# Optimization experiments

Hardware: AMD Instinct MI355X
Metric: run time of the kernel (lower is better)

## Reference

```python
import jax, jax.numpy as jnp
import numpy as np

D, T, B, DEPTH, WIN, H = 1024, 2048, 4, 2, 128, 4
HD = D // H


def setup_inputs() -> dict:
    key = jax.random.key(0)
    ks = iter(jax.random.split(key, 32))
    s = D ** -0.5
    inp = {
        'x': jax.random.normal(next(ks), (B, T, D), jnp.float32),
        'ln1_s': jnp.ones((DEPTH, D)), 'ln1_b': jnp.zeros((DEPTH, D)),
        'ln2_s': jnp.ones((DEPTH, D)), 'ln2_b': jnp.zeros((DEPTH, D)),
        'ln3_s': jnp.ones((DEPTH, D)), 'ln3_b': jnp.zeros((DEPTH, D)),
        'rg_in_w': jax.random.normal(next(ks), (DEPTH, D, D)) * s,
        'rg_in_b': jnp.zeros((DEPTH, D)),
        'rg_gate_w': jax.random.normal(next(ks), (DEPTH, D, D)) * s,
        'rg_gate_b': jnp.zeros((DEPTH, D)),
        'rg_out_w': jax.random.normal(next(ks), (DEPTH, D, D)) * s,
        'rg_out_b': jnp.zeros((DEPTH, D)),
        'qkv_w': jax.random.normal(next(ks), (DEPTH, D, 3 * D)) * s,
        'qkv_b': jnp.zeros((DEPTH, 3 * D)),
        'attn_out_w': jax.random.normal(next(ks), (DEPTH, D, D)) * s,
        'attn_out_b': jnp.zeros((DEPTH, D)),
        'mlp_w1': jax.random.normal(next(ks), (DEPTH, D, 4 * D)) * s,
        'mlp_b1': jnp.zeros((DEPTH, 4 * D)),
        'mlp_w2': jax.random.normal(next(ks), (DEPTH, 4 * D, D)) * (4 * D) ** -0.5,
        'mlp_b2': jnp.zeros((DEPTH, D)),
    }
    return inp


def _ln(x, s, b):
    m = x.mean(-1, keepdims=True)
    v = ((x - m) ** 2).mean(-1, keepdims=True)
    return (x - m) / jnp.sqrt(v + 1e-5) * s + b


def _rg_lru(x, wi, bi, wg, bg, wo, bo):
    u = x @ wi + bi                      # [B,T,D]
    g = jax.nn.sigmoid(x @ wg + bg)      # [B,T,D]
    # h_t = g_t * h_{t-1} + (1-g_t) * u_t, h_{-1}=0 -> log-depth associative scan
    def comb(l, r):
        return (l[0] * r[0], r[0] * l[1] + r[1])
    _, h = jax.lax.associative_scan(comb, (g, (1.0 - g) * u), axis=1)
    return h @ wo + bo


def _local_attn(x, wqkv, bqkv, wo, bo):
    b, t, d = x.shape
    qkv = (x @ wqkv + bqkv).reshape(b, t, 3, H, HD)
    qkv = jnp.transpose(qkv, (2, 0, 3, 1, 4))  # [3,B,H,T,hd]
    q, k, v = qkv[0], qkv[1], qkv[2]
    scores = jnp.einsum('bhid,bhjd->bhij', q, k) / (HD ** 0.5)
    i = jnp.arange(t)[:, None]
    j = jnp.arange(t)[None, :]
    mask = (j <= i) & (j >= i - (WIN - 1))
    scores = jnp.where(mask, scores, -jnp.inf)
    p = jax.nn.softmax(scores, axis=-1)
    y = jnp.einsum('bhij,bhjd->bhid', p, v)
    y = jnp.transpose(y, (0, 2, 1, 3)).reshape(b, t, d)
    return y @ wo + bo


def reference(x, ln1_s, ln1_b, ln2_s, ln2_b, ln3_s, ln3_b,
              rg_in_w, rg_in_b, rg_gate_w, rg_gate_b, rg_out_w, rg_out_b,
              qkv_w, qkv_b, attn_out_w, attn_out_b,
              mlp_w1, mlp_b1, mlp_w2, mlp_b2):
    for l in range(DEPTH):
        x = x + _rg_lru(_ln(x, ln1_s[l], ln1_b[l]),
                        rg_in_w[l], rg_in_b[l], rg_gate_w[l], rg_gate_b[l],
                        rg_out_w[l], rg_out_b[l])
        x = x + _local_attn(_ln(x, ln2_s[l], ln2_b[l]),
                            qkv_w[l], qkv_b[l], attn_out_w[l], attn_out_b[l])
        h = _ln(x, ln3_s[l], ln3_b[l])
        h = jax.nn.gelu(h @ mlp_w1[l] + mlp_b1[l], approximate=False) @ mlp_w2[l] + mlp_b2[l]
        x = x + h
    return x
```

## Files before the change

### kernel.cpp

```cpp
#include <hip/hip_runtime.h>
#include <math.h>

#define DD 1024
#define TT 2048
#define BB 4
#define HH 4
#define HDIM 256
#define NLAYER 2
#define MM (BB*TT)
#define NCHUNK 32
#define CHUNK (TT/NCHUNK)

typedef unsigned short u16;
typedef __bf16 bf16x8 __attribute__((ext_vector_type(8)));
typedef float f32x4 __attribute__((ext_vector_type(4)));

__device__ __forceinline__ float b2f(u16 h) {
  unsigned u = ((unsigned)h) << 16;
  return __builtin_bit_cast(float, u);
}
__device__ __forceinline__ u16 f2b(float f) {
  unsigned u = __builtin_bit_cast(unsigned, f);
  u += 0x7fffu + ((u >> 16) & 1u);
  return (u16)(u >> 16);
}

#define GLD16(g, l) __builtin_amdgcn_global_load_lds( \
    (__attribute__((address_space(1))) void*)(void*)(g), \
    (__attribute__((address_space(3))) void*)(l), 16, 0, 0)

__device__ __forceinline__ void wg_barrier() {
  asm volatile("" ::: "memory");
  __builtin_amdgcn_s_barrier();
  asm volatile("" ::: "memory");
}
template<int N> __device__ __forceinline__ void wait_vmcnt() {
  asm volatile("s_waitcnt vmcnt(%0)" :: "i"(N) : "memory");
}

__global__ __launch_bounds__(256)
void transpose_cvt(const float* __restrict__ W, u16* __restrict__ Wt, int K, int N,
                   size_t lsrc, size_t ldst) {
  __shared__ float tile[32][33];
  const float* Wl = W + (size_t)blockIdx.z * lsrc;
  u16* Wtl = Wt + (size_t)blockIdx.z * ldst;
  const int n0 = blockIdx.x << 5, k0 = blockIdx.y << 5;
  const int tx = threadIdx.x, ty = threadIdx.y;
#pragma unroll
  for (int i = 0; i < 4; ++i)
    tile[ty + i*8][tx] = Wl[(size_t)(k0 + ty + i*8) * N + n0 + tx];
  __syncthreads();
#pragma unroll
  for (int i = 0; i < 4; ++i)
    Wtl[(size_t)(n0 + ty + i*8) * K + k0 + tx] = f2b(tile[tx][ty + i*8]);
}

__global__ __launch_bounds__(256)
void ln_k(const float* __restrict__ x, const float* __restrict__ sc,
          const float* __restrict__ bi, u16* __restrict__ xn) {
  const int row = blockIdx.x;
  const int tid = threadIdx.x;
  const float4 xv = ((const float4*)(x + (size_t)row * DD))[tid];
  float s = xv.x + xv.y + xv.z + xv.w;
  float q = xv.x*xv.x + xv.y*xv.y + xv.z*xv.z + xv.w*xv.w;
#pragma unroll
  for (int o = 1; o < 64; o <<= 1) { s += __shfl_xor(s, o); q += __shfl_xor(q, o); }
  __shared__ float rs[4], rq[4];
  if ((tid & 63) == 0) { rs[tid >> 6] = s; rq[tid >> 6] = q; }
  __syncthreads();
  s = rs[0] + rs[1] + rs[2] + rs[3];
  q = rq[0] + rq[1] + rq[2] + rq[3];
  const float mean = s * (1.f / DD);
  const float var = q * (1.f / DD) - mean * mean;
  const float rstd = rsqrtf(var + 1e-5f);
  const float4 sv = ((const float4*)sc)[tid];
  const float4 bv = ((const float4*)bi)[tid];
  const u16 o0 = f2b((xv.x - mean) * rstd * sv.x + bv.x);
  const u16 o1 = f2b((xv.y - mean) * rstd * sv.y + bv.y);
  const u16 o2 = f2b((xv.z - mean) * rstd * sv.z + bv.z);
  const u16 o3 = f2b((xv.w - mean) * rstd * sv.w + bv.w);
  uint2 pk;
  pk.x = (unsigned)o0 | ((unsigned)o1 << 16);
  pk.y = (unsigned)o2 | ((unsigned)o3 << 16);
  *(uint2*)(xn + (size_t)row * DD + (tid << 2)) = pk;
}

template<int EPI>
__global__ __launch_bounds__(512, 4)
void gemm256t(const u16* __restrict__ A, const u16* __restrict__ Wt,
              const float* __restrict__ bias, const float* __restrict__ bias2,
              float* __restrict__ outf, u16* __restrict__ outb, int K, int N) {
  extern __shared__ u16 lds[];
  const int tid = threadIdx.x;
  const int gx = gridDim.x;
  const int nwg = gx * (int)gridDim.y;
  int lid = (int)blockIdx.y * gx + (int)blockIdx.x;
  lid = (lid & 7) * (nwg >> 3) + (lid >> 3);
  const int m0 = (lid / gx) << 8;
  const int n0 = (lid % gx) << 7;
  const int lane = tid & 63;
  const int wid = tid >> 6;
  const int wm = wid >> 2;
  const int wn = wid & 3;
  const int g = lane >> 4;
  const int lc = lane & 15;
  const int q = tid >> 2;
  const int slot = tid & 3;
  const int scs = (slot ^ ((q >> 1) & 3)) << 3;
  const int so = (g ^ ((lc >> 1) & 3)) << 3;

  u16* Ab = lds;
  u16* Bbase = lds + 24576;
  u16 *Ac = Ab, *An = Ab + 8192, *Aw = Ab + 16384;
  u16 *Bc = Bbase, *Bn = Bbase + 4096, *Bw = Bbase + 8192;

  auto stage = [&](int kt, u16* At, u16* Bt) {
    const int kb = (kt << 5) + scs;
    GLD16(A + (size_t)(m0 + q) * K + kb,       At + q*32 + slot*8);
    GLD16(A + (size_t)(m0 + 128 + q) * K + kb, At + (128 + q)*32 + slot*8);
    GLD16(Wt + (size_t)(n0 + q) * K + kb,      Bt + q*32 + slot*8);
  };

  f32x4 acc[8][2];
#pragma unroll
  for (int i = 0; i < 8; ++i)
#pragma unroll
    for (int j = 0; j < 2; ++j)
#pragma unroll
      for (int e = 0; e < 4; ++e) acc[i][j][e] = 0.f;

  const int KT = K >> 5;
  stage(0, Ac, Bc);
  stage(1, An, Bn);

  for (int kt = 0; kt < KT; ++kt) {
    if (kt + 1 < KT) wait_vmcnt<3>();
    else             wait_vmcnt<0>();
    wg_barrier();
    bf16x8 bf0 = *(const bf16x8*)(Bc + (wn*32 + lc)*32 + so);
    bf16x8 bf1 = *(const bf16x8*)(Bc + (wn*32 + 16 + lc)*32 + so);
    bf16x8 af[8];
#pragma unroll
    for (int i = 0; i < 8; ++i)
      af[i] = *(const bf16x8*)(Ac + (wm*128 + i*16 + lc)*32 + so);
    if (kt + 2 < KT) stage(kt + 2, Aw, Bw);
    __builtin_amdgcn_s_setprio(1);
#pragma unroll
    for (int i = 0; i < 8; ++i) {
      acc[i][0] = __builtin_amdgcn_mfma_f32_16x16x32_bf16(af[i], bf0, acc[i][0], 0, 0, 0);
      acc[i][1] = __builtin_amdgcn_mfma_f32_16x16x32_bf16(af[i], bf1, acc[i][1], 0, 0, 0);
    }
    __builtin_amdgcn_s_setprio(0);
    u16* t;
    t = Ac; Ac = An; An = Aw; Aw = t;
    t = Bc; Bc = Bn; Bn = Bw; Bw = t;
  }

#pragma unroll
  for (int mi = 0; mi < 8; ++mi) {
#pragma unroll
    for (int ni = 0; ni < 2; ++ni) {
      const int n = n0 + wn*32 + ni*16 + lc;
      const int mbase = m0 + wm*128 + mi*16 + (g << 2);
      if (EPI == 4) {
        const float bia = bias[n];
        if (n < 2048) {
#pragma unroll
          for (int e = 0; e < 4; ++e)
            outb[(size_t)(mbase + e) * 2048 + n] = f2b(acc[mi][ni][e] + bia);
        } else {
          const int hh = (n - 2048) >> 8, dim = (n - 2048) & 255;
          const int bidx = mbase >> 11, t = mbase & 2047;
          const u16 a0 = f2b(acc[mi][ni][0] + bia);
          const u16 a1 = f2b(acc[mi][ni][1] + bia);
          const u16 a2 = f2b(acc[mi][ni][2] + bia);
          const u16 a3 = f2b(acc[mi][ni][3] + bia);
          uint2 pk;
          pk.x = (unsigned)a0 | ((unsigned)a1 << 16);
          pk.y = (unsigned)a2 | ((unsigned)a3 << 16);
          u16* vtp = (u16*)outf;
          *(uint2*)(vtp + ((size_t)((bidx*4 + hh)*256 + dim)) * 2048 + t) = pk;
        }
      } else if (EPI == 5) {
        const float bia = (n < 1024) ? bias[n] : bias2[n - 1024];
        u16* dst = (n < 1024) ? outb : (u16*)outf;
        const int nn = n & 1023;
#pragma unroll
        for (int e = 0; e < 4; ++e)
          dst[(size_t)(mbase + e) * 1024 + nn] = f2b(acc[mi][ni][e] + bia);
      } else if (EPI == 2) {
        const float bia = bias[n];
#pragma unroll
        for (int e = 0; e < 4; ++e) {
          const float v = acc[mi][ni][e] + bia;
          const float zc = fminf(fmaxf(1.5957691216f * (v + 0.044715f*v*v*v), -30.f), 30.f);
          outb[(size_t)(mbase + e) * N + n] = f2b(v / (1.f + __expf(-zc)));
        }
      } else {
        const float bia = bias[n];
#pragma unroll
        for (int e = 0; e < 4; ++e)
          outf[(size_t)(mbase + e) * N + n] += acc[mi][ni][e] + bia;
      }
    }
  }
}

__global__ __launch_bounds__(256)
void scan1_k(const u16* __restrict__ zpre, const u16* __restrict__ u,
             float* __restrict__ aggA, float* __restrict__ aggB) {
  const int d = blockIdx.x * 256 + threadIdx.x;
  const int c = blockIdx.y, b = blockIdx.z;
  const size_t base = ((size_t)b * TT + (size_t)c * CHUNK) * DD + d;
  float a = 1.f, acc = 0.f;
  for (int t = 0; t < CHUNK; ++t) {
    const float gl = 1.f / (1.f + __expf(-b2f(zpre[base + (size_t)t * DD])));
    const float ul = b2f(u[base + (size_t)t * DD]);
    acc = gl * acc + (1.f - gl) * ul;
    a *= gl;
  }
  const size_t o = ((size_t)b * NCHUNK + c) * DD + d;
  aggA[o] = a; aggB[o] = acc;
}

__global__ __launch_bounds__(256)
void scan2_k(const float* __restrict__ aggA, const float* __restrict__ aggB,
             float* __restrict__ carry) {
  const int idx = blockIdx.x * 256 + threadIdx.x;
  const int b = idx >> 10, d = idx & 1023;
  float h = 0.f;
  for (int c = 0; c < NCHUNK; ++c) {
    const size_t o = ((size_t)b * NCHUNK + c) * DD + d;
    carry[o] = h;
    h = aggA[o] * h + aggB[o];
  }
}

__global__ __launch_bounds__(256)
void scan3_k(const u16* __restrict__ zpre, const u16* __restrict__ u,
             const float* __restrict__ carry, u16* __restrict__ hout) {
  const int d = blockIdx.x * 256 + threadIdx.x;
  const int c = blockIdx.y, b = blockIdx.z;
  const size_t base = ((size_t)b * TT + (size_t)c * CHUNK) * DD + d;
  float h = carry[((size_t)b * NCHUNK + c) * DD + d];
  for (int t = 0; t < CHUNK; ++t) {
    const float gl = 1.f / (1.f + __expf(-b2f(zpre[base + (size_t)t * DD])));
    const float ul = b2f(u[base + (size_t)t * DD]);
    h = gl * h + (1.f - gl) * ul;
    hout[base + (size_t)t * DD] = f2b(h);
  }
}

__global__ __launch_bounds__(256)
void attn_mfma(const u16* __restrict__ qkb, const u16* __restrict__ vt,
               u16* __restrict__ y) {
  __shared__ u16 kv[16384];
  __shared__ u16 pb[4][16][200];
  const int tid = threadIdx.x;
  const int lane = tid & 63;
  const int wid = tid >> 6;
  const int g = lane >> 4;
  const int lc = lane & 15;
  const int t0 = blockIdx.x << 6;
  const int bh = blockIdx.y;
  const int bT = (bh >> 2) * TT;
  const int h = bh & 3;

  bf16x8 afq[8];
  {
    const u16* qg = qkb + (size_t)(bT + t0 + wid*16 + lc) * 2048 + h*256 + g*8;
#pragma unroll
    for (int ks = 0; ks < 8; ++ks)
      afq[ks] = __builtin_bit_cast(bf16x8, *(const uint4*)(qg + ks*32));
  }

  f32x4 sc[12];
#pragma unroll
  for (int f = 0; f < 12; ++f)
#pragma unroll
    for (int e = 0; e < 4; ++e) sc[f][e] = 0.f;

  const int koff = 1024 + h*256;
#pragma unroll
  for (int c = 0; c < 3; ++c) {
    const int j0 = t0 + (c - 2) * 64;
    if (j0 < 0) {
#pragma unroll
      for (int nt = 0; nt < 4; ++nt)
#pragma unroll
        for (int e = 0; e < 4; ++e) sc[c*4+nt][e] = -1e30f;
      continue;
    }
    __syncthreads();
    {
      const u16* kg = qkb + (size_t)(bT + j0) * 2048 + koff;
#pragma unroll
      for (int i = 0; i < 8; ++i) {
        const int o16 = i*256 + tid;
        const int slab = o16 >> 8, key = (o16 >> 2) & 63, ds = o16 & 3;
        GLD16(kg + (size_t)key*2048 + slab*32 + ds*8, kv + o16*8);
      }
    }
    __syncthreads();
#pragma unroll
    for (int nt = 0; nt < 4; ++nt) {
      f32x4 s = sc[c*4+nt];
#pragma unroll
      for (int ks = 0; ks < 8; ++ks) {
        const bf16x8 kb = *(const bf16x8*)(kv + ks*2048 + (nt*16 + lc)*32 + g*8);
        s = __builtin_amdgcn_mfma_f32_16x16x32_bf16(afq[ks], kb, s, 0, 0, 0);
      }
      sc[c*4+nt] = s;
    }
#pragma unroll
    for (int nt = 0; nt < 4; ++nt)
#pragma unroll
      for (int e = 0; e < 4; ++e) {
        const int tl = wid*16 + g*4 + e;
        const int jl = nt*16 + lc;
        const bool ok = (c == 1) || (c == 2 ? (jl <= tl) : (jl >= tl + 1));
        sc[c*4+nt][e] = ok ? sc[c*4+nt][e] * 0.0625f : -1e30f;
      }
  }

#pragma unroll
  for (int e = 0; e < 4; ++e) {
    float m = -1e30f;
#pragma unroll
    for (int f = 0; f < 12; ++f) m = fmaxf(m, sc[f][e]);
    m = fmaxf(m, __shfl_xor(m, 1)); m = fmaxf(m, __shfl_xor(m, 2));
    m = fmaxf(m, __shfl_xor(m, 4)); m = fmaxf(m, __shfl_xor(m, 8));
    float s = 0.f;
#pragma unroll
    for (int f = 0; f < 12; ++f) { const float p = __expf(sc[f][e] - m); sc[f][e] = p; s += p; }
    s += __shfl_xor(s, 1); s += __shfl_xor(s, 2);
    s += __shfl_xor(s, 4); s += __shfl_xor(s, 8);
    const float is = 1.f / s;
#pragma unroll
    for (int f = 0; f < 12; ++f) sc[f][e] *= is;
  }
#pragma unroll
  for (int c = 0; c < 3; ++c)
#pragma unroll
    for (int nt = 0; nt < 4; ++nt)
#pragma unroll
      for (int e = 0; e < 4; ++e)
        pb[wid][g*4 + e][c*64 + nt*16 + lc] = f2b(sc[c*4+nt][e]);

  f32x4 acc[16];
#pragma unroll
  for (int nt = 0; nt < 16; ++nt)
#pragma unroll
    for (int e = 0; e < 4; ++e) acc[nt][e] = 0.f;

  const u16* vg = vt + (size_t)bh * 256 * 2048;
#pragma unroll
  for (int c = 0; c < 3; ++c) {
    const int j0 = t0 + (c - 2) * 64;
    if (j0 < 0) continue;
    __syncthreads();
#pragma unroll
    for (int i = 0; i < 8; ++i) {
      const int o16 = i*256 + tid;
      const int dim = o16 >> 3, slot = o16 & 7;
      const int ss = slot ^ (dim & 7);
      GLD16(vg + (size_t)dim*2048 + j0 + ss*8, kv + o16*8);
    }
    __syncthreads();
#pragma unroll
    for (int ks = 0; ks < 2; ++ks) {
      const bf16x8 pa = *(const bf16x8*)&pb[wid][lc][(c*2 + ks)*32 + g*8];
#pragma unroll
      for (int nt = 0; nt < 16; ++nt) {
        const int dim = nt*16 + lc;
        int boff = dim*128 + ks*64 + g*16;
        boff ^= (dim & 7) << 4;
        const bf16x8 vb = *(const bf16x8*)((const char*)kv + boff);
        acc[nt] = __builtin_amdgcn_mfma_f32_16x16x32_bf16(pa, vb, acc[nt], 0, 0, 0);
      }
    }
  }

#pragma unroll
  for (int nt = 0; nt < 16; ++nt)
#pragma unroll
    for (int e = 0; e < 4; ++e) {
      const int tok = bT + t0 + wid*16 + g*4 + e;
      y[(size_t)tok * 1024 + h*256 + nt*16 + lc] = f2b(acc[nt][e]);
    }
}

extern "C" void kernel_launch(void* const* d_in, const int* in_sizes, int n_in,
                              void* d_out, int out_size, void* d_ws, size_t ws_size,
                              hipStream_t stream) {
  const float* x_in      = (const float*)d_in[0];
  const float* ln1_s     = (const float*)d_in[1];
  const float* ln1_b     = (const float*)d_in[2];
  const float* ln2_s     = (const float*)d_in[3];
  const float* ln2_b     = (const float*)d_in[4];
  const float* ln3_s     = (const float*)d_in[5];
  const float* ln3_b     = (const float*)d_in[6];
  const float* rg_in_w   = (const float*)d_in[7];
  const float* rg_in_b   = (const float*)d_in[8];
  const float* rg_gate_w = (const float*)d_in[9];
  const float* rg_gate_b = (const float*)d_in[10];
  const float* rg_out_w  = (const float*)d_in[11];
  const float* rg_out_b  = (const float*)d_in[12];
  const float* qkv_w     = (const float*)d_in[13];
  const float* qkv_b     = (const float*)d_in[14];
  const float* attn_out_w= (const float*)d_in[15];
  const float* attn_out_b= (const float*)d_in[16];
  const float* mlp_w1    = (const float*)d_in[17];
  const float* mlp_b1    = (const float*)d_in[18];
  const float* mlp_w2    = (const float*)d_in[19];
  const float* mlp_b2    = (const float*)d_in[20];

  hipFuncSetAttribute((const void*)&gemm256t<5>, hipFuncAttributeMaxDynamicSharedMemorySize, 73728);
  hipFuncSetAttribute((const void*)&gemm256t<4>, hipFuncAttributeMaxDynamicSharedMemorySize, 73728);
  hipFuncSetAttribute((const void*)&gemm256t<2>, hipFuncAttributeMaxDynamicSharedMemorySize, 73728);
  hipFuncSetAttribute((const void*)&gemm256t<3>, hipFuncAttributeMaxDynamicSharedMemorySize, 73728);

  float* x = (float*)d_out;
  char* ws = (char*)d_ws;
  u16*  wt     = (u16*)ws;
  u16*  xn     = (u16*)(ws + 62914560);
  char* bigS   = ws + 62914560 + 16777216;
  char* smallS = bigS + 67108864;
  float* aggA  = (float*)(smallS + 16777216);
  float* aggB  = aggA + (size_t)BB * NCHUNK * DD;
  float* carry = aggB + (size_t)BB * NCHUNK * DD;

  u16* ubuf = (u16*)bigS;
  u16* zbuf = (u16*)(bigS + 33554432);
  u16* qkb  = (u16*)bigS;
  u16* vtb  = (u16*)(bigS + 33554432);
  u16* hid  = (u16*)bigS;
  u16* hbuf = (u16*)smallS;
  u16* ybuf = (u16*)smallS;

  hipMemcpyAsync(x, x_in, (size_t)MM * DD * sizeof(float), hipMemcpyDeviceToDevice, stream);

  const size_t LW = 15728640;
  const dim3 tb(32, 8);
  transpose_cvt<<<dim3(32, 32, 2),  tb, 0, stream>>>(rg_in_w,    wt + 0,        DD, DD,   DD*DD,   LW);
  transpose_cvt<<<dim3(32, 32, 2),  tb, 0, stream>>>(rg_gate_w,  wt + 1048576,  DD, DD,   DD*DD,   LW);
  transpose_cvt<<<dim3(32, 32, 2),  tb, 0, stream>>>(rg_out_w,   wt + 2097152,  DD, DD,   DD*DD,   LW);
  transpose_cvt<<<dim3(96, 32, 2),  tb, 0, stream>>>(qkv_w,      wt + 3145728,  DD, 3072, DD*3072, LW);
  transpose_cvt<<<dim3(32, 32, 2),  tb, 0, stream>>>(attn_out_w, wt + 6291456,  DD, DD,   DD*DD,   LW);
  transpose_cvt<<<dim3(128, 32, 2), tb, 0, stream>>>(mlp_w1,     wt + 7340032,  DD, 4096, DD*4096, LW);
  transpose_cvt<<<dim3(32, 128, 2), tb, 0, stream>>>(mlp_w2,     wt + 11534336, 4096, DD, 4096*DD, LW);

  for (int l = 0; l < NLAYER; ++l) {
    u16* base = wt + (size_t)l * LW;
    ln_k<<<MM, 256, 0, stream>>>(x, ln1_s + l*DD, ln1_b + l*DD, xn);
    gemm256t<5><<<dim3(16, 32), 512, 73728, stream>>>(xn, base + 0, rg_in_b + l*DD, rg_gate_b + l*DD,
                                                      (float*)zbuf, ubuf, DD, 2048);
    scan1_k<<<dim3(4, NCHUNK, BB), 256, 0, stream>>>(zbuf, ubuf, aggA, aggB);
    scan2_k<<<16, 256, 0, stream>>>(aggA, aggB, carry);
    scan3_k<<<dim3(4, NCHUNK, BB), 256, 0, stream>>>(zbuf, ubuf, carry, hbuf);
    gemm256t<3><<<dim3(8, 32), 512, 73728, stream>>>(hbuf, base + 2097152, rg_out_b + l*DD, nullptr,
                                                     x, nullptr, DD, 1024);
    ln_k<<<MM, 256, 0, stream>>>(x, ln2_s + l*DD, ln2_b + l*DD, xn);
    gemm256t<4><<<dim3(24, 32), 512, 73728, stream>>>(xn, base + 3145728, qkv_b + l*3072, nullptr,
                                                      (float*)vtb, qkb, DD, 3072);
    attn_mfma<<<dim3(TT/64, BB*HH), 256, 0, stream>>>(qkb, vtb, ybuf);
    gemm256t<3><<<dim3(8, 32), 512, 73728, stream>>>(ybuf, base + 6291456, attn_out_b + l*DD, nullptr,
                                                     x, nullptr, DD, 1024);
    ln_k<<<MM, 256, 0, stream>>>(x, ln3_s + l*DD, ln3_b + l*DD, xn);
    gemm256t<2><<<dim3(32, 32), 512, 73728, stream>>>(xn, base + 7340032, mlp_b1 + l*4096, nullptr,
                                                      nullptr, hid, DD, 4096);
    gemm256t<3><<<dim3(8, 32), 512, 73728, stream>>>(hid, base + 11534336, mlp_b2 + l*DD, nullptr,
                                                     x, nullptr, 4096, 1024);
  }
}
```

Baseline: 899.6 us.

## Switch GEMM to 32x32x16 MFMA tiles and fuse input copy into residual epilogue

The GEMM warp tiling changes from 16x16x32 MFMAs (each wave covering 128x32) to 32x32x16 MFMAs with each wave covering a 64x64 sub-tile. This cuts LDS fragment loads per MFMA and uses a new XOR swizzle to avoid bank conflicts. The initial device-to-device copy of x is removed: layer 0 reads x_in directly, and the residual epilogue computes out = addf + acc + bias. The epilogue store pattern changes and needs careful correctness on the swizzle.

```diff
diff --git a/kernel.cpp b/kernel.cpp
--- a/kernel.cpp
+++ b/kernel.cpp
@@ -14,6 +14,7 @@
 typedef unsigned short u16;
 typedef __bf16 bf16x8 __attribute__((ext_vector_type(8)));
 typedef float f32x4 __attribute__((ext_vector_type(4)));
+typedef float f32x16 __attribute__((ext_vector_type(16)));
 
 __device__ __forceinline__ float b2f(u16 h) {
   unsigned u = ((unsigned)h) << 16;
@@ -89,6 +90,7 @@
 __global__ __launch_bounds__(512, 4)
 void gemm256t(const u16* __restrict__ A, const u16* __restrict__ Wt,
               const float* __restrict__ bias, const float* __restrict__ bias2,
+              const float* __restrict__ addf,
               float* __restrict__ outf, u16* __restrict__ outb, int K, int N) {
   extern __shared__ u16 lds[];
   const int tid = threadIdx.x;
@@ -100,14 +102,15 @@
   const int n0 = (lid % gx) << 7;
   const int lane = tid & 63;
   const int wid = tid >> 6;
-  const int wm = wid >> 2;
-  const int wn = wid & 3;
-  const int g = lane >> 4;
-  const int lc = lane & 15;
+  const int wm = wid >> 1;
+  const int wn = wid & 1;
+  const int lr = lane & 31;
+  const int lh = lane >> 5;
+  const int Kl = ((lr >> 1) & 3) ^ ((lr >> 3) & 1);
   const int q = tid >> 2;
   const int slot = tid & 3;
-  const int scs = (slot ^ ((q >> 1) & 3)) << 3;
-  const int so = (g ^ ((lc >> 1) & 3)) << 3;
+  const int Kq = ((q >> 1) & 3) ^ ((q >> 3) & 1);
+  const int scs = (slot ^ Kq) << 3;
 
   u16* Ab = lds;
   u16* Bbase = lds + 24576;
@@ -121,13 +124,9 @@
     GLD16(Wt + (size_t)(n0 + q) * K + kb,      Bt + q*32 + slot*8);
   };
 
-  f32x4 acc[8][2];
-#pragma unroll
-  for (int i = 0; i < 8; ++i)
-#pragma unroll
-    for (int j = 0; j < 2; ++j)
-#pragma unroll
-      for (int e = 0; e < 4; ++e) acc[i][j][e] = 0.f;
+  f32x16 accA, accB, accC, accD;
+#pragma unroll
+  for (int e = 0; e < 16; ++e) { accA[e] = 0.f; accB[e] = 0.f; accC[e] = 0.f; accD[e] = 0.f; }
 
   const int KT = K >> 5;
   stage(0, Ac, Bc);
@@ -137,18 +136,25 @@
     if (kt + 1 < KT) wait_vmcnt<3>();
     else             wait_vmcnt<0>();
     wg_barrier();
-    bf16x8 bf0 = *(const bf16x8*)(Bc + (wn*32 + lc)*32 + so);
-    bf16x8 bf1 = *(const bf16x8*)(Bc + (wn*32 + 16 + lc)*32 + so);
-    bf16x8 af[8];
-#pragma unroll
-    for (int i = 0; i < 8; ++i)
-      af[i] = *(const bf16x8*)(Ac + (wm*128 + i*16 + lc)*32 + so);
+    bf16x8 af[2][2], bfr[2][2];
+#pragma unroll
+    for (int mt = 0; mt < 2; ++mt)
+#pragma unroll
+      for (int ks = 0; ks < 2; ++ks)
+        af[mt][ks] = *(const bf16x8*)(Ac + (wm*64 + mt*32 + lr)*32 + (((ks*2 + lh) ^ Kl) << 3));
+#pragma unroll
+    for (int nt = 0; nt < 2; ++nt)
+#pragma unroll
+      for (int ks = 0; ks < 2; ++ks)
+        bfr[nt][ks] = *(const bf16x8*)(Bc + (wn*64 + nt*32 + lr)*32 + (((ks*2 + lh) ^ Kl) << 3));
     if (kt + 2 < KT) stage(kt + 2, Aw, Bw);
     __builtin_amdgcn_s_setprio(1);
 #pragma unroll
-    for (int i = 0; i < 8; ++i) {
-      acc[i][0] = __builtin_amdgcn_mfma_f32_16x16x32_bf16(af[i], bf0, acc[i][0], 0, 0, 0);
-      acc[i][1] = __builtin_amdgcn_mfma_f32_16x16x32_bf16(af[i], bf1, acc[i][1], 0, 0, 0);
+    for (int ks = 0; ks < 2; ++ks) {
+      accA = __builtin_amdgcn_mfma_f32_32x32x16_bf16(af[0][ks], bfr[0][ks], accA, 0, 0, 0);
+      accB = __builtin_amdgcn_mfma_f32_32x32x16_bf16(af[0][ks], bfr[1][ks], accB, 0, 0, 0);
+      accC = __builtin_amdgcn_mfma_f32_32x32x16_bf16(af[1][ks], bfr[0][ks], accC, 0, 0, 0);
+      accD = __builtin_amdgcn_mfma_f32_32x32x16_bf16(af[1][ks], bfr[1][ks], accD, 0, 0, 0);
     }
     __builtin_amdgcn_s_setprio(0);
     u16* t;
@@ -157,50 +163,56 @@
   }
 
 #pragma unroll
-  for (int mi = 0; mi < 8; ++mi) {
-#pragma unroll
-    for (int ni = 0; ni < 2; ++ni) {
-      const int n = n0 + wn*32 + ni*16 + lc;
-      const int mbase = m0 + wm*128 + mi*16 + (g << 2);
-      if (EPI == 4) {
-        const float bia = bias[n];
-        if (n < 2048) {
+  for (int mt = 0; mt < 2; ++mt) {
+#pragma unroll
+    for (int nt = 0; nt < 2; ++nt) {
+      const f32x16 acc = (mt == 0) ? (nt == 0 ? accA : accB) : (nt == 0 ? accC : accD);
+      const int mrow0 = m0 + wm*64 + mt*32;
+      const int n = n0 + wn*64 + nt*32 + lr;
+      const float bia = (EPI == 5) ? ((n & 1024) ? bias2[n & 1023] : bias[n])
+                                   : bias[n];
+#pragma unroll
+      for (int rq = 0; rq < 4; ++rq) {
+        const int rl = 8*rq + 4*lh;
+        if (EPI == 4) {
+          if (n < 2048) {
+#pragma unroll
+            for (int e = 0; e < 4; ++e)
+              outb[(size_t)(mrow0 + rl + e) * 2048 + n] = f2b(acc[rq*4 + e] + bia);
+          } else {
+            const int hh = (n - 2048) >> 8, dim = (n - 2048) & 255;
+            const int grow = mrow0 + rl;
+            const int bidx = grow >> 11, t0 = grow & 2047;
+            const u16 a0 = f2b(acc[rq*4 + 0] + bia);
+            const u16 a1 = f2b(acc[rq*4 + 1] + bia);
+            const u16 a2 = f2b(acc[rq*4 + 2] + bia);
+            const u16 a3 = f2b(acc[rq*4 + 3] + bia);
+            uint2 pk;
+            pk.x = (unsigned)a0 | ((unsigned)a1 << 16);
+            pk.y = (unsigned)a2 | ((unsigned)a3 << 16);
+            u16* vtp = (u16*)outf;
+            *(uint2*)(vtp + ((size_t)((bidx*4 + hh)*256 + dim)) * 2048 + t0) = pk;
+          }
+        } else if (EPI == 5) {
+          u16* dst = (n & 1024) ? (u16*)outf : outb;
+          const int nn = n & 1023;
 #pragma unroll
           for (int e = 0; e < 4; ++e)
-            outb[(size_t)(mbase + e) * 2048 + n] = f2b(acc[mi][ni][e] + bia);
+            dst[(size_t)(mrow0 + rl + e) * 1024 + nn] = f2b(acc[rq*4 + e] + bia);
+        } else if (EPI == 2) {
+#pragma unroll
+          for (int e = 0; e < 4; ++e) {
+            const float v = acc[rq*4 + e] + bia;
+            const float zc = fminf(fmaxf(1.5957691216f * (v + 0.044715f*v*v*v), -30.f), 30.f);
+            outb[(size_t)(mrow0 + rl + e) * N + n] = f2b(v / (1.f + __expf(-zc)));
+          }
         } else {
-          const int hh = (n - 2048) >> 8, dim = (n - 2048) & 255;
-          const int bidx = mbase >> 11, t = mbase & 2047;
-          const u16 a0 = f2b(acc[mi][ni][0] + bia);
-          const u16 a1 = f2b(acc[mi][ni][1] + bia);
-          const u16 a2 = f2b(acc[mi][ni][2] + bia);
-          const u16 a3 = f2b(acc[mi][ni][3] + bia);
-          uint2 pk;
-          pk.x = (unsigned)a0 | ((unsigned)a1 << 16);
-          pk.y = (unsigned)a2 | ((unsigned)a3 << 16);
-          u16* vtp = (u16*)outf;
-          *(uint2*)(vtp + ((size_t)((bidx*4 + hh)*256 + dim)) * 2048 + t) = pk;
+#pragma unroll
+          for (int e = 0; e < 4; ++e) {
+            const size_t idx = (size_t)(mrow0 + rl + e) * N + n;
+            outf[idx] = addf[idx] + acc[rq*4 + e] + bia;
+          }
         }
-      } else if (EPI == 5) {
-        const float bia = (n < 1024) ? bias[n] : bias2[n - 1024];
-        u16* dst = (n < 1024) ? outb : (u16*)outf;
-        const int nn = n & 1023;
-#pragma unroll
-        for (int e = 0; e < 4; ++e)
-          dst[(size_t)(mbase + e) * 1024 + nn] = f2b(acc[mi][ni][e] + bia);
-      } else if (EPI == 2) {
-        const float bia = bias[n];
-#pragma unroll
-        for (int e = 0; e < 4; ++e) {
-          const float v = acc[mi][ni][e] + bia;
-          const float zc = fminf(fmaxf(1.5957691216f * (v + 0.044715f*v*v*v), -30.f), 30.f);
-          outb[(size_t)(mbase + e) * N + n] = f2b(v / (1.f + __expf(-zc)));
-        }
-      } else {
-        const float bia = bias[n];
-#pragma unroll
-        for (int e = 0; e < 4; ++e)
-          outf[(size_t)(mbase + e) * N + n] += acc[mi][ni][e] + bia;
       }
     }
   }
@@ -438,8 +450,6 @@
   u16* hbuf = (u16*)smallS;
   u16* ybuf = (u16*)smallS;
 
-  hipMemcpyAsync(x, x_in, (size_t)MM * DD * sizeof(float), hipMemcpyDeviceToDevice, stream);
-
   const size_t LW = 15728640;
   const dim3 tb(32, 8);
   transpose_cvt<<<dim3(32, 32, 2),  tb, 0, stream>>>(rg_in_w,    wt + 0,        DD, DD,   DD*DD,   LW);
@@ -452,24 +462,25 @@
 
   for (int l = 0; l < NLAYER; ++l) {
     u16* base = wt + (size_t)l * LW;
-    ln_k<<<MM, 256, 0, stream>>>(x, ln1_s + l*DD, ln1_b + l*DD, xn);
+    const float* xsrc = (l == 0) ? x_in : x;
+    ln_k<<<MM, 256, 0, stream>>>(xsrc, ln1_s + l*DD, ln1_b + l*DD, xn);
     gemm256t<5><<<dim3(16, 32), 512, 73728, stream>>>(xn, base + 0, rg_in_b + l*DD, rg_gate_b + l*DD,
-                                                      (float*)zbuf, ubuf, DD, 2048);
+                                                      nullptr, (float*)zbuf, ubuf, DD, 2048);
     scan1_k<<<dim3(4, NCHUNK, BB), 256, 0, stream>>>(zbuf, ubuf, aggA, aggB);
     scan2_k<<<16, 256, 0, stream>>>(aggA, aggB, carry);
     scan3_k<<<dim3(4, NCHUNK, BB), 256, 0, stream>>>(zbuf, ubuf, carry, hbuf);
     gemm256t<3><<<dim3(8, 32), 512, 73728, stream>>>(hbuf, base + 2097152, rg_out_b + l*DD, nullptr,
-                                                     x, nullptr, DD, 1024);
+                                                     xsrc, x, nullptr, DD, 1024);
     ln_k<<<MM, 256, 0, stream>>>(x, ln2_s + l*DD, ln2_b + l*DD, xn);
     gemm256t<4><<<dim3(24, 32), 512, 73728, stream>>>(xn, base + 3145728, qkv_b + l*3072, nullptr,
-                                                      (float*)vtb, qkb, DD, 3072);
+                                                      nullptr, (float*)vtb, qkb, DD, 3072);
     attn_mfma<<<dim3(TT/64, BB*HH), 256, 0, stream>>>(qkb, vtb, ybuf);
     gemm256t<3><<<dim3(8, 32), 512, 73728, stream>>>(ybuf, base + 6291456, attn_out_b + l*DD, nullptr,
-                                                     x, nullptr, DD, 1024);
+                                                     x, x, nullptr, DD, 1024);
     ln_k<<<MM, 256, 0, stream>>>(x, ln3_s + l*DD, ln3_b + l*DD, xn);
     gemm256t<2><<<dim3(32, 32), 512, 73728, stream>>>(xn, base + 7340032, mlp_b1 + l*4096, nullptr,
-                                                      nullptr, hid, DD, 4096);
+                                                      nullptr, nullptr, hid, DD, 4096);
     gemm256t<3><<<dim3(8, 32), 512, 73728, stream>>>(hid, base + 11534336, mlp_b2 + l*DD, nullptr,
-                                                     x, nullptr, 4096, 1024);
-  }
-}
+                                                     x, x, nullptr, 4096, 1024);
+  }
+}
```

After: 893.4 us. About the same (-0.7%).

## Use 128x128-tile residual GEMM for N=1024 projections and drop initial copy

Applied to the files above, without the earlier changes.

Adds a dedicated 128x128-tile GEMM with triple-buffered LDS and XCD-aware block remapping for the three N=1024 projections (rg_out, attn_out, mlp_w2). The old 256-wide tile gave only 256 workgroups, and the smaller tile doubles that to 512 for better CU occupancy. The new epilogue reads the residual from a separate source and writes x, so layer 0 can read x_in directly and the initial device-to-device copy is dropped. The trade-off is lower per-tile data reuse and extra fp32 residual reads.

```diff
diff --git a/kernel.cpp b/kernel.cpp
--- a/kernel.cpp
+++ b/kernel.cpp
@@ -188,7 +188,7 @@
 #pragma unroll
         for (int e = 0; e < 4; ++e)
           dst[(size_t)(mbase + e) * 1024 + nn] = f2b(acc[mi][ni][e] + bia);
-      } else if (EPI == 2) {
+      } else {
         const float bia = bias[n];
 #pragma unroll
         for (int e = 0; e < 4; ++e) {
@@ -196,11 +196,94 @@
           const float zc = fminf(fmaxf(1.5957691216f * (v + 0.044715f*v*v*v), -30.f), 30.f);
           outb[(size_t)(mbase + e) * N + n] = f2b(v / (1.f + __expf(-zc)));
         }
-      } else {
-        const float bia = bias[n];
-#pragma unroll
-        for (int e = 0; e < 4; ++e)
-          outf[(size_t)(mbase + e) * N + n] += acc[mi][ni][e] + bia;
+      }
+    }
+  }
+}
+
+__global__ __launch_bounds__(256, 2)
+void gemm128t(const u16* __restrict__ A, const u16* __restrict__ Wt,
+              const float* __restrict__ bias, const float* __restrict__ addf,
+              float* __restrict__ outf, int K, int N) {
+  extern __shared__ u16 lds[];
+  const int tid = threadIdx.x;
+  const int gx = gridDim.x;
+  const int nwg = gx * (int)gridDim.y;
+  int lid = (int)blockIdx.y * gx + (int)blockIdx.x;
+  lid = (lid & 7) * (nwg >> 3) + (lid >> 3);
+  const int m0 = (lid / gx) << 7;
+  const int n0 = (lid % gx) << 7;
+  const int lane = tid & 63;
+  const int wid = tid >> 6;
+  const int wm = wid >> 1;
+  const int wn = wid & 1;
+  const int g = lane >> 4;
+  const int lc = lane & 15;
+  const int q = tid >> 2;
+  const int slot = tid & 3;
+  const int scs = (slot ^ ((q >> 1) & 3)) << 3;
+  const int so = (g ^ ((lc >> 1) & 3)) << 3;
+
+  u16* Ab = lds;
+  u16* Bbase = lds + 12288;
+  u16 *Ac = Ab, *An = Ab + 4096, *Aw = Ab + 8192;
+  u16 *Bc = Bbase, *Bn = Bbase + 4096, *Bw = Bbase + 8192;
+
+  auto stage = [&](int kt, u16* At, u16* Bt) {
+    const int kb = (kt << 5) + scs;
+    GLD16(A + (size_t)(m0 + q) * K + kb,       At + q*32 + slot*8);
+    GLD16(A + (size_t)(m0 + 64 + q) * K + kb,  At + (64 + q)*32 + slot*8);
+    GLD16(Wt + (size_t)(n0 + q) * K + kb,      Bt + q*32 + slot*8);
+    GLD16(Wt + (size_t)(n0 + 64 + q) * K + kb, Bt + (64 + q)*32 + slot*8);
+  };
+
+  f32x4 acc[4][4];
+#pragma unroll
+  for (int i = 0; i < 4; ++i)
+#pragma unroll
+    for (int j = 0; j < 4; ++j)
+#pragma unroll
+      for (int e = 0; e < 4; ++e) acc[i][j][e] = 0.f;
+
+  const int KT = K >> 5;
+  stage(0, Ac, Bc);
+  stage(1, An, Bn);
+
+  for (int kt = 0; kt < KT; ++kt) {
+    if (kt + 1 < KT) wait_vmcnt<4>();
+    else             wait_vmcnt<0>();
+    wg_barrier();
+    bf16x8 af[4], bfr[4];
+#pragma unroll
+    for (int i = 0; i < 4; ++i)
+      af[i] = *(const bf16x8*)(Ac + (wm*64 + i*16 + lc)*32 + so);
+#pragma unroll
+    for (int j = 0; j < 4; ++j)
+      bfr[j] = *(const bf16x8*)(Bc + (wn*64 + j*16 + lc)*32 + so);
+    if (kt + 2 < KT) stage(kt + 2, Aw, Bw);
+    __builtin_amdgcn_s_setprio(1);
+#pragma unroll
+    for (int i = 0; i < 4; ++i)
+#pragma unroll
+      for (int j = 0; j < 4; ++j)
+        acc[i][j] = __builtin_amdgcn_mfma_f32_16x16x32_bf16(af[i], bfr[j], acc[i][j], 0, 0, 0);
+    __builtin_amdgcn_s_setprio(0);
+    u16* t;
+    t = Ac; Ac = An; An = Aw; Aw = t;
+    t = Bc; Bc = Bn; Bn = Bw; Bw = t;
+  }
+
+#pragma unroll
+  for (int mi = 0; mi < 4; ++mi) {
+#pragma unroll
+    for (int ni = 0; ni < 4; ++ni) {
+      const int n = n0 + wn*64 + ni*16 + lc;
+      const int mbase = m0 + wm*64 + mi*16 + (g << 2);
+      const float bia = bias[n];
+#pragma unroll
+      for (int e = 0; e < 4; ++e) {
+        const size_t idx = (size_t)(mbase + e) * N + n;
+        outf[idx] = addf[idx] + acc[mi][ni][e] + bia;
       }
     }
   }
@@ -418,7 +501,7 @@
   hipFuncSetAttribute((const void*)&gemm256t<5>, hipFuncAttributeMaxDynamicSharedMemorySize, 73728);
   hipFuncSetAttribute((const void*)&gemm256t<4>, hipFuncAttributeMaxDynamicSharedMemorySize, 73728);
   hipFuncSetAttribute((const void*)&gemm256t<2>, hipFuncAttributeMaxDynamicSharedMemorySize, 73728);
-  hipFuncSetAttribute((const void*)&gemm256t<3>, hipFuncAttributeMaxDynamicSharedMemorySize, 73728);
+  hipFuncSetAttribute((const void*)&gemm128t,    hipFuncAttributeMaxDynamicSharedMemorySize, 49152);
 
   float* x = (float*)d_out;
   char* ws = (char*)d_ws;
@@ -438,8 +521,6 @@
   u16* hbuf = (u16*)smallS;
   u16* ybuf = (u16*)smallS;
 
-  hipMemcpyAsync(x, x_in, (size_t)MM * DD * sizeof(float), hipMemcpyDeviceToDevice, stream);
-
   const size_t LW = 15728640;
   const dim3 tb(32, 8);
   transpose_cvt<<<dim3(32, 32, 2),  tb, 0, stream>>>(rg_in_w,    wt + 0,        DD, DD,   DD*DD,   LW);
@@ -452,24 +533,25 @@
 
   for (int l = 0; l < NLAYER; ++l) {
     u16* base = wt + (size_t)l * LW;
-    ln_k<<<MM, 256, 0, stream>>>(x, ln1_s + l*DD, ln1_b + l*DD, xn);
+    const float* xsrc = (l == 0) ? x_in : x;
+    ln_k<<<MM, 256, 0, stream>>>(xsrc, ln1_s + l*DD, ln1_b + l*DD, xn);
     gemm256t<5><<<dim3(16, 32), 512, 73728, stream>>>(xn, base + 0, rg_in_b + l*DD, rg_gate_b + l*DD,
                                                       (float*)zbuf, ubuf, DD, 2048);
     scan1_k<<<dim3(4, NCHUNK, BB), 256, 0, stream>>>(zbuf, ubuf, aggA, aggB);
     scan2_k<<<16, 256, 0, stream>>>(aggA, aggB, carry);
     scan3_k<<<dim3(4, NCHUNK, BB), 256, 0, stream>>>(zbuf, ubuf, carry, hbuf);
-    gemm256t<3><<<dim3(8, 32), 512, 73728, stream>>>(hbuf, base + 2097152, rg_out_b + l*DD, nullptr,
-                                                     x, nullptr, DD, 1024);
+    gemm128t<<<dim3(8, 64), 256, 49152, stream>>>(hbuf, base + 2097152, rg_out_b + l*DD,
+                                                  xsrc, x, DD, 1024);
     ln_k<<<MM, 256, 0, stream>>>(x, ln2_s + l*DD, ln2_b + l*DD, xn);
     gemm256t<4><<<dim3(24, 32), 512, 73728, stream>>>(xn, base + 3145728, qkv_b + l*3072, nullptr,
                                                       (float*)vtb, qkb, DD, 3072);
     attn_mfma<<<dim3(TT/64, BB*HH), 256, 0, stream>>>(qkb, vtb, ybuf);
-    gemm256t<3><<<dim3(8, 32), 512, 73728, stream>>>(ybuf, base + 6291456, attn_out_b + l*DD, nullptr,
-                                                     x, nullptr, DD, 1024);
+    gemm128t<<<dim3(8, 64), 256, 49152, stream>>>(ybuf, base + 6291456, attn_out_b + l*DD,
+                                                  x, x, DD, 1024);
     ln_k<<<MM, 256, 0, stream>>>(x, ln3_s + l*DD, ln3_b + l*DD, xn);
     gemm256t<2><<<dim3(32, 32), 512, 73728, stream>>>(xn, base + 7340032, mlp_b1 + l*4096, nullptr,
                                                       nullptr, hid, DD, 4096);
-    gemm256t<3><<<dim3(8, 32), 512, 73728, stream>>>(hid, base + 11534336, mlp_b2 + l*DD, nullptr,
-                                                     x, nullptr, 4096, 1024);
-  }
-}
+    gemm128t<<<dim3(8, 64), 256, 49152, stream>>>(hid, base + 11534336, mlp_b2 + l*DD,
+                                                  x, x, 4096, 1024);
+  }
+}
```

After: 848.2 us. 5.7% less time.

## Shrink GEMM tile to 128x128 with 4 waves and fold input copy into residual

Applied to the files above, without the earlier changes.

Replaces the 256x128 GEMM tile with 8 waves by a 128x128 tile with 4 waves, each wave computing a 64x64 sub-tile with 4x4 MFMAs. This uses less LDS, doubles the number of workgroups and allows more blocks per CU, which should improve load balance on the many-CU device. It also drops the upfront device-to-device copy of x: the first layer reads x_in directly, and the residual epilogue writes out = addf + acc instead of accumulating in place. The smaller tile reloads more operand data per FLOP, which raises global and LDS traffic.

```diff
diff --git a/kernel.cpp b/kernel.cpp
--- a/kernel.cpp
+++ b/kernel.cpp
@@ -86,9 +86,10 @@
 }
 
 template<int EPI>
-__global__ __launch_bounds__(512, 4)
-void gemm256t(const u16* __restrict__ A, const u16* __restrict__ Wt,
+__global__ __launch_bounds__(256, 3)
+void gemm128t(const u16* __restrict__ A, const u16* __restrict__ Wt,
               const float* __restrict__ bias, const float* __restrict__ bias2,
+              const float* __restrict__ addf,
               float* __restrict__ outf, u16* __restrict__ outb, int K, int N) {
   extern __shared__ u16 lds[];
   const int tid = threadIdx.x;
@@ -96,12 +97,12 @@
   const int nwg = gx * (int)gridDim.y;
   int lid = (int)blockIdx.y * gx + (int)blockIdx.x;
   lid = (lid & 7) * (nwg >> 3) + (lid >> 3);
-  const int m0 = (lid / gx) << 8;
+  const int m0 = (lid / gx) << 7;
   const int n0 = (lid % gx) << 7;
   const int lane = tid & 63;
   const int wid = tid >> 6;
-  const int wm = wid >> 2;
-  const int wn = wid & 3;
+  const int wm = wid >> 1;
+  const int wn = wid & 1;
   const int g = lane >> 4;
   const int lc = lane & 15;
   const int q = tid >> 2;
@@ -110,22 +111,23 @@
   const int so = (g ^ ((lc >> 1) & 3)) << 3;
 
   u16* Ab = lds;
-  u16* Bbase = lds + 24576;
-  u16 *Ac = Ab, *An = Ab + 8192, *Aw = Ab + 16384;
+  u16* Bbase = lds + 12288;
+  u16 *Ac = Ab, *An = Ab + 4096, *Aw = Ab + 8192;
   u16 *Bc = Bbase, *Bn = Bbase + 4096, *Bw = Bbase + 8192;
 
   auto stage = [&](int kt, u16* At, u16* Bt) {
     const int kb = (kt << 5) + scs;
     GLD16(A + (size_t)(m0 + q) * K + kb,       At + q*32 + slot*8);
-    GLD16(A + (size_t)(m0 + 128 + q) * K + kb, At + (128 + q)*32 + slot*8);
+    GLD16(A + (size_t)(m0 + 64 + q) * K + kb,  At + (64 + q)*32 + slot*8);
     GLD16(Wt + (size_t)(n0 + q) * K + kb,      Bt + q*32 + slot*8);
+    GLD16(Wt + (size_t)(n0 + 64 + q) * K + kb, Bt + (64 + q)*32 + slot*8);
   };
 
-  f32x4 acc[8][2];
-#pragma unroll
-  for (int i = 0; i < 8; ++i)
-#pragma unroll
-    for (int j = 0; j < 2; ++j)
+  f32x4 acc[4][4];
+#pragma unroll
+  for (int i = 0; i < 4; ++i)
+#pragma unroll
+    for (int j = 0; j < 4; ++j)
 #pragma unroll
       for (int e = 0; e < 4; ++e) acc[i][j][e] = 0.f;
 
@@ -134,22 +136,23 @@
   stage(1, An, Bn);
 
   for (int kt = 0; kt < KT; ++kt) {
-    if (kt + 1 < KT) wait_vmcnt<3>();
+    if (kt + 1 < KT) wait_vmcnt<4>();
     else             wait_vmcnt<0>();
     wg_barrier();
-    bf16x8 bf0 = *(const bf16x8*)(Bc + (wn*32 + lc)*32 + so);
-    bf16x8 bf1 = *(const bf16x8*)(Bc + (wn*32 + 16 + lc)*32 + so);
-    bf16x8 af[8];
-#pragma unroll
-    for (int i = 0; i < 8; ++i)
-      af[i] = *(const bf16x8*)(Ac + (wm*128 + i*16 + lc)*32 + so);
+    bf16x8 af[4], bfr[4];
+#pragma unroll
+    for (int i = 0; i < 4; ++i)
+      af[i] = *(const bf16x8*)(Ac + (wm*64 + i*16 + lc)*32 + so);
+#pragma unroll
+    for (int j = 0; j < 4; ++j)
+      bfr[j] = *(const bf16x8*)(Bc + (wn*64 + j*16 + lc)*32 + so);
     if (kt + 2 < KT) stage(kt + 2, Aw, Bw);
     __builtin_amdgcn_s_setprio(1);
 #pragma unroll
-    for (int i = 0; i < 8; ++i) {
-      acc[i][0] = __builtin_amdgcn_mfma_f32_16x16x32_bf16(af[i], bf0, acc[i][0], 0, 0, 0);
-      acc[i][1] = __builtin_amdgcn_mfma_f32_16x16x32_bf16(af[i], bf1, acc[i][1], 0, 0, 0);
-    }
+    for (int i = 0; i < 4; ++i)
+#pragma unroll
+      for (int j = 0; j < 4; ++j)
+        acc[i][j] = __builtin_amdgcn_mfma_f32_16x16x32_bf16(af[i], bfr[j], acc[i][j], 0, 0, 0);
     __builtin_amdgcn_s_setprio(0);
     u16* t;
     t = Ac; Ac = An; An = Aw; Aw = t;
@@ -157,11 +160,11 @@
   }
 
 #pragma unroll
-  for (int mi = 0; mi < 8; ++mi) {
-#pragma unroll
-    for (int ni = 0; ni < 2; ++ni) {
-      const int n = n0 + wn*32 + ni*16 + lc;
-      const int mbase = m0 + wm*128 + mi*16 + (g << 2);
+  for (int mi = 0; mi < 4; ++mi) {
+#pragma unroll
+    for (int ni = 0; ni < 4; ++ni) {
+      const int n = n0 + wn*64 + ni*16 + lc;
+      const int mbase = m0 + wm*64 + mi*16 + (g << 2);
       if (EPI == 4) {
         const float bia = bias[n];
         if (n < 2048) {
@@ -199,8 +202,10 @@
       } else {
         const float bia = bias[n];
 #pragma unroll
-        for (int e = 0; e < 4; ++e)
-          outf[(size_t)(mbase + e) * N + n] += acc[mi][ni][e] + bia;
+        for (int e = 0; e < 4; ++e) {
+          const size_t idx = (size_t)(mbase + e) * N + n;
+          outf[idx] = addf[idx] + acc[mi][ni][e] + bia;
+        }
       }
     }
   }
@@ -415,10 +420,10 @@
   const float* mlp_w2    = (const float*)d_in[19];
   const float* mlp_b2    = (const float*)d_in[20];
 
-  hipFuncSetAttribute((const void*)&gemm256t<5>, hipFuncAttributeMaxDynamicSharedMemorySize, 73728);
-  hipFuncSetAttribute((const void*)&gemm256t<4>, hipFuncAttributeMaxDynamicSharedMemorySize, 73728);
-  hipFuncSetAttribute((const void*)&gemm256t<2>, hipFuncAttributeMaxDynamicSharedMemorySize, 73728);
-  hipFuncSetAttribute((const void*)&gemm256t<3>, hipFuncAttributeMaxDynamicSharedMemorySize, 73728);
+  hipFuncSetAttribute((const void*)&gemm128t<2>, hipFuncAttributeMaxDynamicSharedMemorySize, 49152);
+  hipFuncSetAttribute((const void*)&gemm128t<3>, hipFuncAttributeMaxDynamicSharedMemorySize, 49152);
+  hipFuncSetAttribute((const void*)&gemm128t<4>, hipFuncAttributeMaxDynamicSharedMemorySize, 49152);
+  hipFuncSetAttribute((const void*)&gemm128t<5>, hipFuncAttributeMaxDynamicSharedMemorySize, 49152);
 
   float* x = (float*)d_out;
   char* ws = (char*)d_ws;
@@ -438,8 +443,6 @@
   u16* hbuf = (u16*)smallS;
   u16* ybuf = (u16*)smallS;
 
-  hipMemcpyAsync(x, x_in, (size_t)MM * DD * sizeof(float), hipMemcpyDeviceToDevice, stream);
-
   const size_t LW = 15728640;
   const dim3 tb(32, 8);
   transpose_cvt<<<dim3(32, 32, 2),  tb, 0, stream>>>(rg_in_w,    wt + 0,        DD, DD,   DD*DD,   LW);
@@ -452,24 +455,25 @@
 
   for (int l = 0; l < NLAYER; ++l) {
     u16* base = wt + (size_t)l * LW;
-    ln_k<<<MM, 256, 0, stream>>>(x, ln1_s + l*DD, ln1_b + l*DD, xn);
-    gemm256t<5><<<dim3(16, 32), 512, 73728, stream>>>(xn, base + 0, rg_in_b + l*DD, rg_gate_b + l*DD,
-                                                      (float*)zbuf, ubuf, DD, 2048);
+    const float* xsrc = (l == 0) ? x_in : x;
+    ln_k<<<MM, 256, 0, stream>>>(xsrc, ln1_s + l*DD, ln1_b + l*DD, xn);
+    gemm128t<5><<<dim3(16, 64), 256, 49152, stream>>>(xn, base + 0, rg_in_b + l*DD, rg_gate_b + l*DD,
+                                                      nullptr, (float*)zbuf, ubuf, DD, 2048);
     scan1_k<<<dim3(4, NCHUNK, BB), 256, 0, stream>>>(zbuf, ubuf, aggA, aggB);
     scan2_k<<<16, 256, 0, stream>>>(aggA, aggB, carry);
     scan3_k<<<dim3(4, NCHUNK, BB), 256, 0, stream>>>(zbuf, ubuf, carry, hbuf);
-    gemm256t<3><<<dim3(8, 32), 512, 73728, stream>>>(hbuf, base + 2097152, rg_out_b + l*DD, nullptr,
-                                                     x, nullptr, DD, 1024);
+    gemm128t<3><<<dim3(8, 64), 256, 49152, stream>>>(hbuf, base + 2097152, rg_out_b + l*DD, nullptr,
+                                                     xsrc, x, nullptr, DD, 1024);
     ln_k<<<MM, 256, 0, stream>>>(x, ln2_s + l*DD, ln2_b + l*DD, xn);
-    gemm256t<4><<<dim3(24, 32), 512, 73728, stream>>>(xn, base + 3145728, qkv_b + l*3072, nullptr,
-                                                      (float*)vtb, qkb, DD, 3072);
+    gemm128t<4><<<dim3(24, 64), 256, 49152, stream>>>(xn, base + 3145728, qkv_b + l*3072, nullptr,
+                                                      nullptr, (float*)vtb, qkb, DD, 3072);
     attn_mfma<<<dim3(TT/64, BB*HH), 256, 0, stream>>>(qkb, vtb, ybuf);
-    gemm256t<3><<<dim3(8, 32), 512, 73728, stream>>>(ybuf, base + 6291456, attn_out_b + l*DD, nullptr,
-                                                     x, nullptr, DD, 1024);
+    gemm128t<3><<<dim3(8, 64), 256, 49152, stream>>>(ybuf, base + 6291456, attn_out_b + l*DD, nullptr,
+                                                     x, x, nullptr, DD, 1024);
     ln_k<<<MM, 256, 0, stream>>>(x, ln3_s + l*DD, ln3_b + l*DD, xn);
-    gemm256t<2><<<dim3(32, 32), 512, 73728, stream>>>(xn, base + 7340032, mlp_b1 + l*4096, nullptr,
-                                                      nullptr, hid, DD, 4096);
-    gemm256t<3><<<dim3(8, 32), 512, 73728, stream>>>(hid, base + 11534336, mlp_b2 + l*DD, nullptr,
-                                                     x, nullptr, 4096, 1024);
-  }
-}
+    gemm128t<2><<<dim3(32, 64), 256, 49152, stream>>>(xn, base + 7340032, mlp_b1 + l*4096, nullptr,
+                                                      nullptr, nullptr, hid, DD, 4096);
+    gemm128t<3><<<dim3(8, 64), 256, 49152, stream>>>(hid, base + 11534336, mlp_b2 + l*DD, nullptr,
+                                                     x, x, nullptr, 4096, 1024);
+  }
+}
```

Measured after the change: 897.0 us. No clear change (-0.3%).
